# Optimization experiments

Hardware: AMD Instinct MI355X
Metric: run time of the kernel (lower is better)

## Reference

```python
import jax, jax.numpy as jnp
import numpy as np

# Dims: B nodes, Z species (elements), IN/OUT channels, M = 2*l+1 (l=1)
B, Z, IN, OUT, M = 8192, 10, 512, 512, 3
ALPHA = 1.0 / np.sqrt(IN)  # self.alpha = 1/sqrt(in_dim)
SQRT3 = float(np.sqrt(3.0))


def setup_inputs() -> dict:
    key = jax.random.key(0)
    k1, k2, k3 = jax.random.split(key, 3)
    t = jax.random.normal(k1, (B, IN, M), dtype=jnp.float32)
    species = jax.random.randint(k2, (B,), 0, Z)
    node_attrs = jax.nn.one_hot(species, Z, dtype=jnp.float32)  # [B, Z] one-hot
    # torch.nn.init.uniform_(weights, -sqrt(3), sqrt(3))
    weights = jax.random.uniform(k3, (Z, OUT, IN), dtype=jnp.float32,
                                 minval=-SQRT3, maxval=SQRT3)
    return {"t": t, "node_attrs": node_attrs, "weights": weights}


def reference(t, node_attrs, weights):
    # Faithful to: einsum('bz, zCc, bcd -> bCd', node_attrs, weights*alpha, t)
    # Contract weights with t first per species ([Z,B,C,M], ~500MB), which
    # avoids the huge [B,C,c] per-node weight-gather intermediate, then
    # select/sum over species with the one-hot node_attrs.
    W = weights * ALPHA                       # [Z, OUT, IN]
    zt = jnp.einsum('zCc,bcd->zbCd', W, t)    # [Z, B, OUT, M]
    out = jnp.einsum('bz,zbCd->bCd', node_attrs, zt)  # [B, OUT, M]
    return out
```

## Files before the change

### kernel.cpp

```cpp
#include <hip/hip_runtime.h>
#include <stdint.h>

#define NB   8192
#define NZ   10
#define CIN  512
#define COUT 512
#define MM   3
#define ALPHA 0.04419417382415922f

#define ROWS_TOTAL (NB * MM)
#define BM 128
#define BN 128
#define BK 32
#define KITERS (CIN / BK)
#define MAX_MT (ROWS_TOTAL / BM + NZ)
#define NYB (COUT / BN)
#define NWG (MAX_MT * NYB)
#define NGRP 32

typedef short bf16x8 __attribute__((ext_vector_type(8)));
typedef float f32x4  __attribute__((ext_vector_type(4)));

__device__ __forceinline__ uint16_t f2bf(float f) {
    union { float f; uint32_t i; } v; v.f = f;
    uint32_t x = v.i;
    x += 0x7fffu + ((x >> 16) & 1u);
    return (uint16_t)(x >> 16);
}
__device__ __forceinline__ uint32_t pack2(float a, float b) {
    return (uint32_t)f2bf(a) | ((uint32_t)f2bf(b) << 16);
}
__device__ __forceinline__ void async16(const void* g, void* l) {
    __builtin_amdgcn_global_load_lds((const uint32_t*)g, (uint32_t*)l, 16, 0, 0);
}

__global__ __launch_bounds__(256)
void prep_kernel(const float* __restrict__ attrs, const float* __restrict__ w,
                 int* __restrict__ species, int* __restrict__ hist,
                 ushort* __restrict__ wt) {
    const int tid = threadIdx.x;
    if (blockIdx.x >= NGRP) {
        const size_t base = (size_t)(blockIdx.x - NGRP) * 2048;
        const float* src = w + base;
        ushort* dst = wt + base;
        float4 a = *(const float4*)(src + tid * 4);
        float4 b = *(const float4*)(src + 1024 + tid * 4);
        uint2 oa, ob;
        oa.x = pack2(a.x, a.y); oa.y = pack2(a.z, a.w);
        ob.x = pack2(b.x, b.y); ob.y = pack2(b.z, b.w);
        *(uint2*)(dst + tid * 4) = oa;
        *(uint2*)(dst + 1024 + tid * 4) = ob;
        return;
    }
    __shared__ int wc[4][NZ];
    const int b = blockIdx.x * 256 + tid;
    const float* a = attrs + (size_t)b * NZ;
    int s = 0;
    #pragma unroll
    for (int z = 0; z < NZ; z++) if (a[z] > 0.5f) s = z;
    species[b] = s;
    const int wv = tid >> 6, lane = tid & 63;
    #pragma unroll
    for (int z = 0; z < NZ; z++) {
        unsigned long long m = __ballot(s == z);
        if (lane == 0) wc[wv][z] = __popcll(m);
    }
    __syncthreads();
    if (tid < NZ) {
        hist[blockIdx.x * NZ + tid] = wc[0][tid] + wc[1][tid] + wc[2][tid] + wc[3][tid];
    }
}

__global__ __launch_bounds__(256)
void place_kernel(const int* __restrict__ species, const int* __restrict__ hist,
                  int* __restrict__ sorted, int* __restrict__ offsets,
                  int* __restrict__ tile_offsets) {
    __shared__ int lhist[NGRP][NZ];
    __shared__ int loff[NZ + 1], ltoff[NZ + 1];
    __shared__ int pb[NZ];
    __shared__ int wc[4][NZ];
    const int tid = threadIdx.x, g = blockIdx.x;

    for (int i = tid; i < NGRP * NZ; i += 256) ((int*)lhist)[i] = hist[i];
    __syncthreads();
    if (tid == 0) {
        int off = 0, toff = 0;
        for (int z = 0; z < NZ; z++) {
            int tot = 0;
            for (int gg = 0; gg < NGRP; gg++) tot += lhist[gg][z];
            loff[z] = off; ltoff[z] = toff;
            off += tot;
            toff += (3 * tot + BM - 1) / BM;
        }
        loff[NZ] = off; ltoff[NZ] = toff;
    }
    __syncthreads();
    if (tid < NZ) {
        int base = loff[tid];
        for (int gg = 0; gg < g; gg++) base += lhist[gg][tid];
        pb[tid] = base;
    }
    if (g == 0 && tid < NZ + 1) {
        offsets[tid] = loff[tid];
        tile_offsets[tid] = ltoff[tid];
    }
    const int b = g * 256 + tid;
    const int s = species[b];
    const int wv = tid >> 6, lane = tid & 63;
    unsigned long long mymask = 0;
    #pragma unroll
    for (int z = 0; z < NZ; z++) {
        unsigned long long m = __ballot(s == z);
        if (lane == 0) wc[wv][z] = __popcll(m);
        if (s == z) mymask = m;
    }
    __syncthreads();
    int rank = __popcll(mymask & ((1ull << lane) - 1ull));
    #pragma unroll
    for (int w2 = 0; w2 < 4; w2++) if (w2 < wv) rank += wc[w2][s];
    sorted[pb[s] + rank] = b;
}

__global__ __launch_bounds__(256)
void pack_t(const float* __restrict__ t, const int* __restrict__ sorted,
            ushort* __restrict__ tt) {
    const int w = threadIdx.x >> 6, L = threadIdx.x & 63;
    const int p = blockIdx.x * 4 + w;
    const int node = sorted[p];
    const float4* src = (const float4*)(t + (size_t)node * (CIN * MM) + L * 24);
    float4 f[6];
    #pragma unroll
    for (int i = 0; i < 6; i++) f[i] = src[i];
    const float* v = (const float*)f;
    #pragma unroll
    for (int d = 0; d < MM; d++) {
        uint4 o;
        o.x = pack2(v[d],      v[3 + d]);
        o.y = pack2(v[6 + d],  v[9 + d]);
        o.z = pack2(v[12 + d], v[15 + d]);
        o.w = pack2(v[18 + d], v[21 + d]);
        *(uint4*)&tt[(size_t)(3 * p + d) * CIN + L * 8] = o;
    }
}

__global__ __launch_bounds__(256)
void gemm_kernel(const ushort* __restrict__ tt, const ushort* __restrict__ wt,
                 const int* __restrict__ sorted, const int* __restrict__ offsets,
                 const int* __restrict__ tile_offsets, float* __restrict__ out) {
    __shared__ __align__(16) ushort smem[3][2][BM][BK];
    __shared__ int spos[48];

    const int bid = blockIdx.x;
    const int nid = (bid & 7) * (NWG / 8) + (bid >> 3);
    const int tz = nid >> 2;
    const int Cbase = (nid & 3) * BN;

    if (tz >= tile_offsets[NZ]) return;
    int z = 0;
    #pragma unroll
    for (int i = 1; i < NZ; i++) if (tile_offsets[i] <= tz) z = i;

    const int row_base = 3 * offsets[z] + (tz - tile_offsets[z]) * BM;
    const int row_end  = 3 * offsets[z + 1];
    const int pos0     = row_base / 3;

    const int tid = threadIdx.x;
    const int w = tid >> 6, L = tid & 63;
    if (tid < 48) spos[tid] = sorted[min(pos0 + tid, NB - 1)];

    const int lr = L >> 2;
    const int cs = (L & 3) ^ ((L >> 3) & 3);
    const int soff = lr * CIN + cs * 8;
    const ushort* gA = tt + (size_t)(row_base + w * 32) * CIN + soff;
    const ushort* gB = wt + ((size_t)z * COUT + Cbase + w * 32) * CIN + soff;

    const int wm = w & 1, wn = w >> 1;
    const int q = L >> 4, mr = L & 15;
    const int sr8 = (q ^ ((mr >> 1) & 3)) * 8;

    f32x4 acc[4][4];
    #pragma unroll
    for (int i = 0; i < 4; i++)
        #pragma unroll
        for (int j = 0; j < 4; j++) acc[i][j] = (f32x4){0.f, 0.f, 0.f, 0.f};

#define STAGE(bufi, ko) do {                                                 \
        async16(gA + (ko),            &smem[bufi][0][w * 32][0]);            \
        async16(gA + 16 * CIN + (ko), &smem[bufi][0][w * 32 + 16][0]);       \
        async16(gB + (ko),            &smem[bufi][1][w * 32][0]);            \
        async16(gB + 16 * CIN + (ko), &smem[bufi][1][w * 32 + 16][0]);       \
    } while (0)

    STAGE(0, 0);
    STAGE(1, BK);
    int cur = 0, nxt = 2;
    for (int kt = 0; kt < KITERS; kt++) {
        if (kt + 1 < KITERS) {
            asm volatile("s_waitcnt vmcnt(4)" ::: "memory");
        } else {
            asm volatile("s_waitcnt vmcnt(0)" ::: "memory");
        }
        asm volatile("s_barrier" ::: "memory");

        if (kt + 2 < KITERS) STAGE(nxt, (kt + 2) * BK);

        bf16x8 af[4], bf[4];
        #pragma unroll
        for (int am = 0; am < 4; am++)
            af[am] = *(const bf16x8*)&smem[cur][0][wm * 64 + am * 16 + mr][sr8];
        #pragma unroll
        for (int bn = 0; bn < 4; bn++)
            bf[bn] = *(const bf16x8*)&smem[cur][1][wn * 64 + bn * 16 + mr][sr8];
        #pragma unroll
        for (int am = 0; am < 4; am++)
            #pragma unroll
            for (int bn = 0; bn < 4; bn++)
                acc[am][bn] = __builtin_amdgcn_mfma_f32_16x16x32_bf16(
                    af[am], bf[bn], acc[am][bn], 0, 0, 0);

        cur = (cur == 2) ? 0 : cur + 1;
        nxt = (nxt == 2) ? 0 : nxt + 1;
    }
#undef STAGE

    float* ebuf = (float*)smem;
    #pragma unroll
    for (int ch = 0; ch < 3; ch++) {
        __syncthreads();
        const int pbase = pos0 + ch * 16;
        #pragma unroll
        for (int am = 0; am < 4; am++) {
            #pragma unroll
            for (int r = 0; r < 4; r++) {
                const int Rg = row_base + wm * 64 + am * 16 + q * 4 + r;
                const int pos = Rg / 3;
                const int d = Rg - 3 * pos;
                const int lp = pos - pbase;
                if (lp >= 0 && lp < 16 && Rg < row_end) {
                    #pragma unroll
                    for (int bn = 0; bn < 4; bn++) {
                        const int c = wn * 64 + bn * 16 + mr;
                        ebuf[(lp * BN + c) * 3 + d] = ALPHA * acc[am][bn][r];
                    }
                }
            }
        }
        __syncthreads();
        #pragma unroll 4
        for (int j = 0; j < 24; j++) {
            const int idx = j * 256 + tid;
            const int lp  = idx / 384;
            const int o   = idx - lp * 384;
            const int pos = pbase + lp;
            const int d   = o % 3;
            const int row = 3 * pos + d;
            if (row >= row_base && row < row_base + BM && row < row_end) {
                const int node = spos[pos - pos0];
                out[(size_t)node * (COUT * MM) + Cbase * 3 + o] = ebuf[idx];
            }
        }
    }
}

extern "C" void kernel_launch(void* const* d_in, const int* in_sizes, int n_in,
                              void* d_out, int out_size, void* d_ws, size_t ws_size,
                              hipStream_t stream) {
    const float* t     = (const float*)d_in[0];
    const float* attrs = (const float*)d_in[1];
    const float* w     = (const float*)d_in[2];
    float* out = (float*)d_out;

    uint8_t* ws = (uint8_t*)d_ws;
    int* species      = (int*)ws;                  ws += NB * 4;
    int* sorted       = (int*)ws;                  ws += NB * 4;
    int* hist         = (int*)ws;                  ws += NGRP * NZ * 4;
    int* offsets      = (int*)ws;                  ws += 16 * 4;
    int* tile_offsets = (int*)ws;                  ws += 16 * 4;
    ws = (uint8_t*)(((uintptr_t)ws + 255) & ~(uintptr_t)255);
    ushort* wt = (ushort*)ws;                      ws += (size_t)NZ * COUT * CIN * 2;
    ushort* tt = (ushort*)ws;

    hipLaunchKernelGGL(prep_kernel, dim3(NGRP + (NZ * COUT * CIN) / 2048), dim3(256),
                       0, stream, attrs, w, species, hist, wt);
    hipLaunchKernelGGL(place_kernel, dim3(NGRP), dim3(256), 0, stream,
                       species, hist, sorted, offsets, tile_offsets);
    hipLaunchKernelGGL(pack_t, dim3(NB / 4), dim3(256), 0, stream, t, sorted, tt);
    hipLaunchKernelGGL(gemm_kernel, dim3(NWG), dim3(256), 0, stream,
                       tt, wt, sorted, offsets, tile_offsets, out);
}
```

Measured before the change: 153.7 us.

## Merge prep, placement and t-packing into one kernel; gather A rows in GEMM

Folds the species histogram, placement and bf16 packing of t into a single prep launch. Each placement block now recomputes the full histogram redundantly instead of using a separate pass. t is packed in original node order, so the GEMM gathers each A row through the sorted index rather than reading a pre-sorted buffer. This drops two kernel launches and their dependency serialization, at the cost of redundant attribute scans and non-contiguous per-row A loads in the GEMM.

```diff
diff --git a/kernel.cpp b/kernel.cpp
--- a/kernel.cpp
+++ b/kernel.cpp
@@ -17,6 +17,9 @@
 #define NYB (COUT / BN)
 #define NWG (MAX_MT * NYB)
 #define NGRP 32
+#define NPW_BLK (NZ * COUT * CIN / 2048)
+#define NPT_BLK (NB / 4)
+#define PREP_BLKS (NGRP + NPW_BLK + NPT_BLK)
 
 typedef short bf16x8 __attribute__((ext_vector_type(8)));
 typedef float f32x4  __attribute__((ext_vector_type(4)));
@@ -35,12 +38,37 @@
 }
 
 __global__ __launch_bounds__(256)
-void prep_kernel(const float* __restrict__ attrs, const float* __restrict__ w,
-                 int* __restrict__ species, int* __restrict__ hist,
-                 ushort* __restrict__ wt) {
-    const int tid = threadIdx.x;
-    if (blockIdx.x >= NGRP) {
-        const size_t base = (size_t)(blockIdx.x - NGRP) * 2048;
+void prep_kernel(const float* __restrict__ t, const float* __restrict__ attrs,
+                 const float* __restrict__ w, int* __restrict__ sorted,
+                 int* __restrict__ offsets, int* __restrict__ tile_offsets,
+                 ushort* __restrict__ wt, ushort* __restrict__ ttn) {
+    __shared__ int wc[4][NZ];
+    __shared__ int cnt_before[NZ], cnt_total[NZ];
+    __shared__ int loff[NZ + 1], ltoff[NZ + 1];
+
+    const int bid = blockIdx.x, tid = threadIdx.x;
+
+    if (bid >= NGRP + NPW_BLK) {
+        const int wv = tid >> 6, L = tid & 63;
+        const int node = (bid - NGRP - NPW_BLK) * 4 + wv;
+        const float4* src = (const float4*)(t + (size_t)node * (CIN * MM) + L * 24);
+        float4 f[6];
+        #pragma unroll
+        for (int i = 0; i < 6; i++) f[i] = src[i];
+        const float* v = (const float*)f;
+        #pragma unroll
+        for (int d = 0; d < MM; d++) {
+            uint4 o;
+            o.x = pack2(v[d],      v[3 + d]);
+            o.y = pack2(v[6 + d],  v[9 + d]);
+            o.z = pack2(v[12 + d], v[15 + d]);
+            o.w = pack2(v[18 + d], v[21 + d]);
+            *(uint4*)&ttn[(size_t)(3 * node + d) * CIN + L * 8] = o;
+        }
+        return;
+    }
+    if (bid >= NGRP) {
+        const size_t base = (size_t)(bid - NGRP) * 2048;
         const float* src = w + base;
         ushort* dst = wt + base;
         float4 a = *(const float4*)(src + tid * 4);
@@ -52,99 +80,60 @@
         *(uint2*)(dst + 1024 + tid * 4) = ob;
         return;
     }
-    __shared__ int wc[4][NZ];
-    const int b = blockIdx.x * 256 + tid;
-    const float* a = attrs + (size_t)b * NZ;
-    int s = 0;
-    #pragma unroll
-    for (int z = 0; z < NZ; z++) if (a[z] > 0.5f) s = z;
-    species[b] = s;
+
+    const int g = bid;
     const int wv = tid >> 6, lane = tid & 63;
-    #pragma unroll
-    for (int z = 0; z < NZ; z++) {
-        unsigned long long m = __ballot(s == z);
-        if (lane == 0) wc[wv][z] = __popcll(m);
-    }
+    if (tid < NZ) { cnt_before[tid] = 0; cnt_total[tid] = 0; }
     __syncthreads();
-    if (tid < NZ) {
-        hist[blockIdx.x * NZ + tid] = wc[0][tid] + wc[1][tid] + wc[2][tid] + wc[3][tid];
-    }
-}
-
-__global__ __launch_bounds__(256)
-void place_kernel(const int* __restrict__ species, const int* __restrict__ hist,
-                  int* __restrict__ sorted, int* __restrict__ offsets,
-                  int* __restrict__ tile_offsets) {
-    __shared__ int lhist[NGRP][NZ];
-    __shared__ int loff[NZ + 1], ltoff[NZ + 1];
-    __shared__ int pb[NZ];
-    __shared__ int wc[4][NZ];
-    const int tid = threadIdx.x, g = blockIdx.x;
-
-    for (int i = tid; i < NGRP * NZ; i += 256) ((int*)lhist)[i] = hist[i];
-    __syncthreads();
+
+    int mys = 0, myrank = 0;
+    for (int cc = 0; cc < NGRP; cc++) {
+        const int n = cc * 256 + tid;
+        const float* a = attrs + (size_t)n * NZ;
+        int s = 0;
+        #pragma unroll
+        for (int z = 0; z < NZ; z++) if (a[z] > 0.5f) s = z;
+        unsigned long long mymask = 0;
+        #pragma unroll
+        for (int z = 0; z < NZ; z++) {
+            unsigned long long m = __ballot(s == z);
+            if (lane == 0) wc[wv][z] = __popcll(m);
+            if (s == z) mymask = m;
+        }
+        __syncthreads();
+        if (tid < NZ) {
+            const int c4 = wc[0][tid] + wc[1][tid] + wc[2][tid] + wc[3][tid];
+            cnt_total[tid] += c4;
+            if (cc < g) cnt_before[tid] += c4;
+        }
+        if (cc == g) {
+            mys = s;
+            int r = __popcll(mymask & ((1ull << lane) - 1ull));
+            #pragma unroll
+            for (int w2 = 0; w2 < 4; w2++) if (w2 < wv) r += wc[w2][s];
+            myrank = r;
+        }
+        __syncthreads();
+    }
     if (tid == 0) {
         int off = 0, toff = 0;
         for (int z = 0; z < NZ; z++) {
-            int tot = 0;
-            for (int gg = 0; gg < NGRP; gg++) tot += lhist[gg][z];
             loff[z] = off; ltoff[z] = toff;
-            off += tot;
-            toff += (3 * tot + BM - 1) / BM;
+            off += cnt_total[z];
+            toff += (3 * cnt_total[z] + BM - 1) / BM;
         }
         loff[NZ] = off; ltoff[NZ] = toff;
     }
     __syncthreads();
-    if (tid < NZ) {
-        int base = loff[tid];
-        for (int gg = 0; gg < g; gg++) base += lhist[gg][tid];
-        pb[tid] = base;
-    }
     if (g == 0 && tid < NZ + 1) {
         offsets[tid] = loff[tid];
         tile_offsets[tid] = ltoff[tid];
     }
-    const int b = g * 256 + tid;
-    const int s = species[b];
-    const int wv = tid >> 6, lane = tid & 63;
-    unsigned long long mymask = 0;
-    #pragma unroll
-    for (int z = 0; z < NZ; z++) {
-        unsigned long long m = __ballot(s == z);
-        if (lane == 0) wc[wv][z] = __popcll(m);
-        if (s == z) mymask = m;
-    }
-    __syncthreads();
-    int rank = __popcll(mymask & ((1ull << lane) - 1ull));
-    #pragma unroll
-    for (int w2 = 0; w2 < 4; w2++) if (w2 < wv) rank += wc[w2][s];
-    sorted[pb[s] + rank] = b;
+    sorted[loff[mys] + cnt_before[mys] + myrank] = g * 256 + tid;
 }
 
 __global__ __launch_bounds__(256)
-void pack_t(const float* __restrict__ t, const int* __restrict__ sorted,
-            ushort* __restrict__ tt) {
-    const int w = threadIdx.x >> 6, L = threadIdx.x & 63;
-    const int p = blockIdx.x * 4 + w;
-    const int node = sorted[p];
-    const float4* src = (const float4*)(t + (size_t)node * (CIN * MM) + L * 24);
-    float4 f[6];
-    #pragma unroll
-    for (int i = 0; i < 6; i++) f[i] = src[i];
-    const float* v = (const float*)f;
-    #pragma unroll
-    for (int d = 0; d < MM; d++) {
-        uint4 o;
-        o.x = pack2(v[d],      v[3 + d]);
-        o.y = pack2(v[6 + d],  v[9 + d]);
-        o.z = pack2(v[12 + d], v[15 + d]);
-        o.w = pack2(v[18 + d], v[21 + d]);
-        *(uint4*)&tt[(size_t)(3 * p + d) * CIN + L * 8] = o;
-    }
-}
-
-__global__ __launch_bounds__(256)
-void gemm_kernel(const ushort* __restrict__ tt, const ushort* __restrict__ wt,
+void gemm_kernel(const ushort* __restrict__ ttn, const ushort* __restrict__ wt,
                  const int* __restrict__ sorted, const int* __restrict__ offsets,
                  const int* __restrict__ tile_offsets, float* __restrict__ out) {
     __shared__ __align__(16) ushort smem[3][2][BM][BK];
@@ -170,9 +159,15 @@
 
     const int lr = L >> 2;
     const int cs = (L & 3) ^ ((L >> 3) & 3);
-    const int soff = lr * CIN + cs * 8;
-    const ushort* gA = tt + (size_t)(row_base + w * 32) * CIN + soff;
-    const ushort* gB = wt + ((size_t)z * COUT + Cbase + w * 32) * CIN + soff;
+    const int R0 = row_base + w * 32 + lr;
+    const int R1 = R0 + 16;
+    const int pA0 = R0 / 3, dA0 = R0 - 3 * pA0;
+    const int pA1 = R1 / 3, dA1 = R1 - 3 * pA1;
+    const int nA0 = sorted[min(pA0, NB - 1)];
+    const int nA1 = sorted[min(pA1, NB - 1)];
+    const ushort* gA0 = ttn + (size_t)(3 * nA0 + dA0) * CIN + cs * 8;
+    const ushort* gA1 = ttn + (size_t)(3 * nA1 + dA1) * CIN + cs * 8;
+    const ushort* gB  = wt + ((size_t)z * COUT + Cbase + w * 32 + lr) * CIN + cs * 8;
 
     const int wm = w & 1, wn = w >> 1;
     const int q = L >> 4, mr = L & 15;
@@ -185,8 +180,8 @@
         for (int j = 0; j < 4; j++) acc[i][j] = (f32x4){0.f, 0.f, 0.f, 0.f};
 
 #define STAGE(bufi, ko) do {                                                 \
-        async16(gA + (ko),            &smem[bufi][0][w * 32][0]);            \
-        async16(gA + 16 * CIN + (ko), &smem[bufi][0][w * 32 + 16][0]);       \
+        async16(gA0 + (ko),           &smem[bufi][0][w * 32][0]);            \
+        async16(gA1 + (ko),           &smem[bufi][0][w * 32 + 16][0]);       \
         async16(gB + (ko),            &smem[bufi][1][w * 32][0]);            \
         async16(gB + 16 * CIN + (ko), &smem[bufi][1][w * 32 + 16][0]);       \
     } while (0)
@@ -271,20 +266,15 @@
     float* out = (float*)d_out;
 
     uint8_t* ws = (uint8_t*)d_ws;
-    int* species      = (int*)ws;                  ws += NB * 4;
     int* sorted       = (int*)ws;                  ws += NB * 4;
-    int* hist         = (int*)ws;                  ws += NGRP * NZ * 4;
     int* offsets      = (int*)ws;                  ws += 16 * 4;
     int* tile_offsets = (int*)ws;                  ws += 16 * 4;
     ws = (uint8_t*)(((uintptr_t)ws + 255) & ~(uintptr_t)255);
-    ushort* wt = (ushort*)ws;                      ws += (size_t)NZ * COUT * CIN * 2;
-    ushort* tt = (ushort*)ws;
-
-    hipLaunchKernelGGL(prep_kernel, dim3(NGRP + (NZ * COUT * CIN) / 2048), dim3(256),
-                       0, stream, attrs, w, species, hist, wt);
-    hipLaunchKernelGGL(place_kernel, dim3(NGRP), dim3(256), 0, stream,
-                       species, hist, sorted, offsets, tile_offsets);
-    hipLaunchKernelGGL(pack_t, dim3(NB / 4), dim3(256), 0, stream, t, sorted, tt);
+    ushort* wt  = (ushort*)ws;                     ws += (size_t)NZ * COUT * CIN * 2;
+    ushort* ttn = (ushort*)ws;
+
+    hipLaunchKernelGGL(prep_kernel, dim3(PREP_BLKS), dim3(256), 0, stream,
+                       t, attrs, w, sorted, offsets, tile_offsets, wt, ttn);
     hipLaunchKernelGGL(gemm_kernel, dim3(NWG), dim3(256), 0, stream,
-                       tt, wt, sorted, offsets, tile_offsets, out);
-}
+                       ttn, wt, sorted, offsets, tile_offsets, out);
+}
```

Result: slower. 173.6 us (+12.9%).
